# Performance work log

Hardware: AMD Instinct MI355X
Metric: run time of the kernel (lower is better)

The kernel has to match this reference:

```python
import jax, jax.numpy as jnp
from jax import lax
import numpy as np

B, T = 8, 65536
IN_CH, OUT_CH = 1, 2
RES_CH, SKIP_CH = 32, 64
KS, DEPTH, STACKS = 3, 8, 2
L = DEPTH * STACKS
DILATIONS = [2 ** (i % DEPTH) for i in range(L)]


def causal_conv1d(x, w, b, dilation=1):
    # x: (B, Cin, T), w: (Cout, Cin, K) -> (B, Cout, T), left-padded causal
    pad = (w.shape[-1] - 1) * dilation
    out = lax.conv_general_dilated(
        x, w, window_strides=(1,), padding=[(pad, 0)],
        rhs_dilation=(dilation,), dimension_numbers=('NCH', 'OIH', 'NCH'))
    return out + b[None, :, None]


def setup_inputs() -> dict:
    key = jax.random.key(0)
    ks = jax.random.split(key, 16)
    s = 0.05  # small init keeps exp(0.5*log_var) well-behaved
    inp = {
        'x': jax.random.normal(ks[0], (B, IN_CH, T), jnp.float32),
        'W_in': jax.random.normal(ks[1], (L, RES_CH, IN_CH, 1), jnp.float32) * s,
        'b_in': jnp.zeros((L, RES_CH), jnp.float32),
        'W_f': jax.random.normal(ks[2], (L, RES_CH, RES_CH, KS), jnp.float32) * s,
        'b_f': jnp.zeros((L, RES_CH), jnp.float32),
        'W_g': jax.random.normal(ks[3], (L, RES_CH, RES_CH, KS), jnp.float32) * s,
        'b_g': jnp.zeros((L, RES_CH), jnp.float32),
        'W_s': jax.random.normal(ks[4], (L, SKIP_CH, RES_CH, 1), jnp.float32) * s,
        'b_s': jnp.zeros((L, SKIP_CH), jnp.float32),
        'W_o': jax.random.normal(ks[5], (L, IN_CH, RES_CH, 1), jnp.float32) * s,
        'b_o': jnp.zeros((L, IN_CH), jnp.float32),
        'W_sk1': jax.random.normal(ks[6], (SKIP_CH, SKIP_CH, 1), jnp.float32) * s,
        'b_sk1': jnp.zeros((SKIP_CH,), jnp.float32),
        'W_sk2': jax.random.normal(ks[7], (OUT_CH, SKIP_CH, 1), jnp.float32) * s,
        'b_sk2': jnp.zeros((OUT_CH,), jnp.float32),
    }
    return inp


def reference(x, W_in, b_in, W_f, b_f, W_g, b_g, W_s, b_s, W_o, b_o,
              W_sk1, b_sk1, W_sk2, b_sk2):
    out = x
    skip_acc = jnp.zeros((x.shape[0], SKIP_CH, x.shape[2]), x.dtype)
    for i in range(L):
        d = DILATIONS[i]
        residual = causal_conv1d(out, W_in[i], b_in[i])           # (B,res,T)
        f = jnp.tanh(causal_conv1d(residual, W_f[i], b_f[i], d))
        g = jax.nn.sigmoid(causal_conv1d(residual, W_g[i], b_g[i], d))
        gated = f * g
        skip_acc = skip_acc + causal_conv1d(gated, W_s[i], b_s[i])
        out = causal_conv1d(gated, W_o[i], b_o[i]) + out
    skip = jax.nn.relu(causal_conv1d(skip_acc, W_sk1, b_sk1))
    output = causal_conv1d(skip, W_sk2, b_sk2)                    # (B,2,T)
    means = output[:, 0, :]
    stds = jnp.exp(0.5 * output[:, 1, :])
    return means, stds
```

## Files before the change

kernel.cpp:

```cpp
#include <hip/hip_runtime.h>
#include <hip/hip_bf16.h>
#include <math.h>

#define T_LEN 65536
#define B_N   8
#define BT    (T_LEN * B_N)
#define L_N   16
#define RC    32
#define SC    64

#define NT1   256
#define CL    512

#define TS    128

#define A_AF0 0
#define A_AF1 32
#define A_AF2 64
#define A_CF0 96
#define A_CF1 128
#define A_BFC 160
#define A_AG0 192
#define A_AG1 224
#define A_AG2 256
#define A_CG0 288
#define A_CG1 320
#define A_BGC 352
#define A_BFI 384
#define A_BGI 416
#define FW_L  448
#define FW_BSUM (L_N * FW_L)
#define FW_F32  (FW_BSUM + 64)
#define WSBF_N  (L_N * SC * RC)
#define W1BF_N  (SC * SC)

typedef float v2f __attribute__((ext_vector_type(2)));
typedef __attribute__((ext_vector_type(4))) float f4;
typedef __attribute__((ext_vector_type(8))) short bf8;

#define MFMA16(a, b, c) __builtin_amdgcn_mfma_f32_16x16x32_bf16(a, b, c, 0, 0, 0)

__device__ __forceinline__ float fast_rcp(float x) { return __builtin_amdgcn_rcpf(x); }

__device__ __forceinline__ float gated_fn(float fp, float gp) {
    float E = __builtin_amdgcn_exp2f(fp);
    float F = __builtin_amdgcn_exp2f(gp);
    return (E - 1.f) * F * fast_rcp((E + 1.f) * (F + 1.f));
}

__device__ __forceinline__ unsigned short f2bf(float f) {
    unsigned u = __float_as_uint(f);
    u += 0x7fffu + ((u >> 16) & 1u);
    return (unsigned short)(u >> 16);
}

__device__ __forceinline__ unsigned pk2(float lo, float hi) {
    __hip_bfloat162 h = __float22bfloat162_rn(make_float2(lo, hi));
    unsigned u; __builtin_memcpy(&u, &h, 4); return u;
}

__device__ __forceinline__ bf8 mk_bf8(unsigned a, unsigned b, unsigned c, unsigned d) {
    unsigned v[4] = {a, b, c, d};
    bf8 r; __builtin_memcpy(&r, v, 16); return r;
}

__global__ __launch_bounds__(256) void prep_kernel(
    const float* __restrict__ W_f, const float* __restrict__ W_g,
    const float* __restrict__ W_in, const float* __restrict__ b_in,
    const float* __restrict__ b_f, const float* __restrict__ b_g,
    const float* __restrict__ b_s, const float* __restrict__ W_s,
    const float* __restrict__ W_sk1, float* __restrict__ fw,
    short* __restrict__ fwh)
{
    const float SF = 2.88539008177792681472f;
    const float SG = 1.44269504088896340736f;
    int idx = blockIdx.x * 256 + threadIdx.x;
    if (idx < L_N * RC) {
        int i = idx >> 5, c = idx & 31;
        float af[3] = {0,0,0}, cf[3] = {0,0,0}, ag[3] = {0,0,0}, cg[3] = {0,0,0};
        for (int cin = 0; cin < RC; ++cin) {
            float wi = W_in[i * RC + cin];
            float bi = b_in[i * RC + cin];
            #pragma unroll
            for (int k = 0; k < 3; ++k) {
                float wf = W_f[((i * RC + c) * RC + cin) * 3 + k];
                float wg = W_g[((i * RC + c) * RC + cin) * 3 + k];
                af[k] = fmaf(wf, wi, af[k]);
                cf[k] = fmaf(wf, bi, cf[k]);
                ag[k] = fmaf(wg, wi, ag[k]);
                cg[k] = fmaf(wg, bi, cg[k]);
            }
        }
        float* p = fw + i * FW_L;
        p[A_AF0 + c] = af[0] * SF; p[A_AF1 + c] = af[1] * SF; p[A_AF2 + c] = af[2] * SF;
        p[A_CF0 + c] = cf[0] * SF; p[A_CF1 + c] = cf[1] * SF;
        p[A_BFC + c] = (b_f[i * RC + c] + cf[2]) * SF;
        p[A_BFI + c] = (b_f[i * RC + c] + cf[2] + cf[0] + cf[1]) * SF;
        p[A_AG0 + c] = ag[0] * SG; p[A_AG1 + c] = ag[1] * SG; p[A_AG2 + c] = ag[2] * SG;
        p[A_CG0 + c] = cg[0] * SG; p[A_CG1 + c] = cg[1] * SG;
        p[A_BGC + c] = (b_g[i * RC + c] + cg[2]) * SG;
        p[A_BGI + c] = (b_g[i * RC + c] + cg[2] + cg[0] + cg[1]) * SG;
    } else if (idx < L_N * RC + SC) {
        int s = idx - L_N * RC;
        float acc = 0.f;
        for (int i = 0; i < L_N; ++i) acc += b_s[i * SC + s];
        fw[FW_BSUM + s] = acc;
    } else if (idx < 576 + WSBF_N) {
        int j = idx - 576;
        fwh[j] = (short)f2bf(W_s[j]);
    } else if (idx < 576 + WSBF_N + W1BF_N) {
        int j = idx - 576 - WSBF_N;
        fwh[WSBF_N + j] = (short)f2bf(W_sk1[j]);
    }
}

__global__ __launch_bounds__(NT1) void layer_kernel(
    const float* __restrict__ src, float* __restrict__ dst,
    const float* __restrict__ gwl, const float* __restrict__ wol,
    const float* __restrict__ bol, int d)
{
    int b     = blockIdx.x >> 7;
    int chunk = blockIdx.x & 127;
    int t0    = chunk * CL;
    const float* sb = src + (size_t)b * T_LEN;
    float*       db = dst + (size_t)b * T_LEN;
    int tid = threadIdx.x;
    int h   = 2 * d;

    int ta = t0 + tid, tb = ta + NT1;
    v2f s2p, s1p, s0p;
    v2f accp = (v2f){0.f, 0.f};

    if (chunk != 0) {
        s2p.x = sb[ta];     s2p.y = sb[tb];
        s1p.x = sb[ta - d]; s1p.y = sb[tb - d];
        s0p.x = sb[ta - h]; s0p.y = sb[tb - h];
        for (int c4 = 0; c4 < 8; ++c4) {
            f4 vaf0 = *(const f4*)(gwl + A_AF0 + c4 * 4);
            f4 vaf1 = *(const f4*)(gwl + A_AF1 + c4 * 4);
            f4 vaf2 = *(const f4*)(gwl + A_AF2 + c4 * 4);
            f4 vbfi = *(const f4*)(gwl + A_BFI + c4 * 4);
            f4 vag0 = *(const f4*)(gwl + A_AG0 + c4 * 4);
            f4 vag1 = *(const f4*)(gwl + A_AG1 + c4 * 4);
            f4 vag2 = *(const f4*)(gwl + A_AG2 + c4 * 4);
            f4 vbgi = *(const f4*)(gwl + A_BGI + c4 * 4);
            f4 vwo  = *(const f4*)(wol + c4 * 4);
            #pragma unroll
            for (int e = 0; e < 4; ++e) {
                float af0 = vaf0[e], af1 = vaf1[e], af2 = vaf2[e], bfi = vbfi[e];
                float ag0 = vag0[e], ag1 = vag1[e], ag2 = vag2[e], bgi = vbgi[e];
                float woc = vwo[e];
                v2f fp = (v2f){bfi, bfi} + s0p * (v2f){af0, af0} + s1p * (v2f){af1, af1} + s2p * (v2f){af2, af2};
                v2f gp = (v2f){bgi, bgi} + s0p * (v2f){ag0, ag0} + s1p * (v2f){ag1, ag1} + s2p * (v2f){ag2, ag2};
                v2f g;
                g.x = gated_fn(fp.x, gp.x);
                g.y = gated_fn(fp.y, gp.y);
                accp = accp + g * (v2f){woc, woc};
            }
        }
    } else {
        v2f m1p, m0p;
        m1p.x = (ta >= d) ? 1.f : 0.f; m1p.y = (tb >= d) ? 1.f : 0.f;
        m0p.x = (ta >= h) ? 1.f : 0.f; m0p.y = (tb >= h) ? 1.f : 0.f;
        s2p.x = sb[ta];
        s2p.y = sb[tb];
        s1p.x = (ta >= d) ? sb[ta - d] : 0.f;
        s1p.y = (tb >= d) ? sb[tb - d] : 0.f;
        s0p.x = (ta >= h) ? sb[ta - h] : 0.f;
        s0p.y = (tb >= h) ? sb[tb - h] : 0.f;
        for (int c4 = 0; c4 < 8; ++c4) {
            f4 vaf0 = *(const f4*)(gwl + A_AF0 + c4 * 4);
            f4 vaf1 = *(const f4*)(gwl + A_AF1 + c4 * 4);
            f4 vaf2 = *(const f4*)(gwl + A_AF2 + c4 * 4);
            f4 vcf0 = *(const f4*)(gwl + A_CF0 + c4 * 4);
            f4 vcf1 = *(const f4*)(gwl + A_CF1 + c4 * 4);
            f4 vbfc = *(const f4*)(gwl + A_BFC + c4 * 4);
            f4 vag0 = *(const f4*)(gwl + A_AG0 + c4 * 4);
            f4 vag1 = *(const f4*)(gwl + A_AG1 + c4 * 4);
            f4 vag2 = *(const f4*)(gwl + A_AG2 + c4 * 4);
            f4 vcg0 = *(const f4*)(gwl + A_CG0 + c4 * 4);
            f4 vcg1 = *(const f4*)(gwl + A_CG1 + c4 * 4);
            f4 vbgc = *(const f4*)(gwl + A_BGC + c4 * 4);
            f4 vwo  = *(const f4*)(wol + c4 * 4);
            #pragma unroll
            for (int e = 0; e < 4; ++e) {
                float af0 = vaf0[e], af1 = vaf1[e], af2 = vaf2[e];
                float cf0 = vcf0[e], cf1 = vcf1[e], bfc = vbfc[e];
                float ag0 = vag0[e], ag1 = vag1[e], ag2 = vag2[e];
                float cg0 = vcg0[e], cg1 = vcg1[e], bgc = vbgc[e];
                float woc = vwo[e];
                v2f fp = (v2f){bfc, bfc} + m0p * (v2f){cf0, cf0} + m1p * (v2f){cf1, cf1};
                fp = fp + s0p * (v2f){af0, af0} + s1p * (v2f){af1, af1} + s2p * (v2f){af2, af2};
                v2f gp = (v2f){bgc, bgc} + m0p * (v2f){cg0, cg0} + m1p * (v2f){cg1, cg1};
                gp = gp + s0p * (v2f){ag0, ag0} + s1p * (v2f){ag1, ag1} + s2p * (v2f){ag2, ag2};
                v2f g;
                g.x = gated_fn(fp.x, gp.x);
                g.y = gated_fn(fp.y, gp.y);
                accp = accp + g * (v2f){woc, woc};
            }
        }
    }
    float bo = *bol;
    db[ta] = s2p.x + bo + accp.x;
    db[tb] = s2p.y + bo + accp.y;
}

#define SMB_W    0
#define SMB_MISC 28672
#define SMB_TOT  29712

__global__ __launch_bounds__(256) void pass2_kernel(
    const float* __restrict__ x, const float* __restrict__ streams,
    const float* __restrict__ fw, const short* __restrict__ Wsbf,
    const short* __restrict__ W1bf, const float* __restrict__ b_sk1,
    const float* __restrict__ W_sk2, const float* __restrict__ b_sk2,
    float* __restrict__ out)
{
    __shared__ __align__(16) char smb[SMB_TOT];
    float* sW    = (float*)smb;
    float* sMisc = (float*)(smb + SMB_MISC);

    int tid   = threadIdx.x;
    int b     = blockIdx.x >> 9;
    int chunk = blockIdx.x & 511;
    int t0    = chunk * TS;

    for (int j = tid; j < (L_N * FW_L) / 4; j += 256)
        ((f4*)sW)[j] = ((const f4*)fw)[j];
    if (tid < 64) { sMisc[tid] = fw[FW_BSUM + tid]; sMisc[64 + tid] = b_sk1[tid]; }
    if (tid < 128) sMisc[128 + tid] = W_sk2[tid];
    if (tid < 2)   sMisc[256 + tid] = b_sk2[tid];
    __syncthreads();

    int wv   = tid >> 6;
    int lane = tid & 63;
    int m    = lane & 15;
    int q    = lane >> 4;

    int tr0 = t0 + wv * 32 + m;
    int tr1 = tr0 + 16;

    f4 zero4 = {0.f, 0.f, 0.f, 0.f};
    f4 acc[2][4];
    #pragma unroll
    for (int tt = 0; tt < 2; ++tt)
        #pragma unroll
        for (int st = 0; st < 4; ++st) acc[tt][st] = zero4;

    const float* xb = x + (size_t)b * T_LEN;
    for (int i = 0; i < L_N; ++i) {
        int d = 1 << (i & 7);
        const float* src = (i == 0) ? xb
                                    : (streams + (size_t)(i - 1) * BT + (size_t)b * T_LEN);
        const float* w = sW + i * FW_L + q * 8;

        bf8 bfrag[4];
        #pragma unroll
        for (int st = 0; st < 4; ++st)
            bfrag[st] = *(const bf8*)(Wsbf + i * (SC * RC) + (st * 16 + m) * RC + q * 8);

        unsigned uf[2][4];
        if (t0 >= 2 * d) {
            float s2a = src[tr0], s1a = src[tr0 - d], s0a = src[tr0 - 2 * d];
            float s2b = src[tr1], s1b = src[tr1 - d], s0b = src[tr1 - 2 * d];
            #pragma unroll
            for (int hc = 0; hc < 2; ++hc) {
                const float* wc = w + hc * 4;
                f4 af0 = *(const f4*)(wc + A_AF0), af1 = *(const f4*)(wc + A_AF1), af2 = *(const f4*)(wc + A_AF2);
                f4 bfi = *(const f4*)(wc + A_BFI);
                f4 ag0 = *(const f4*)(wc + A_AG0), ag1 = *(const f4*)(wc + A_AG1), ag2 = *(const f4*)(wc + A_AG2);
                f4 bgi = *(const f4*)(wc + A_BGI);
                f4 fpa = bfi + s0a * af0 + s1a * af1 + s2a * af2;
                f4 gpa = bgi + s0a * ag0 + s1a * ag1 + s2a * ag2;
                f4 fpb = bfi + s0b * af0 + s1b * af1 + s2b * af2;
                f4 gpb = bgi + s0b * ag0 + s1b * ag1 + s2b * ag2;
                uf[0][hc * 2 + 0] = pk2(gated_fn(fpa[0], gpa[0]), gated_fn(fpa[1], gpa[1]));
                uf[0][hc * 2 + 1] = pk2(gated_fn(fpa[2], gpa[2]), gated_fn(fpa[3], gpa[3]));
                uf[1][hc * 2 + 0] = pk2(gated_fn(fpb[0], gpb[0]), gated_fn(fpb[1], gpb[1]));
                uf[1][hc * 2 + 1] = pk2(gated_fn(fpb[2], gpb[2]), gated_fn(fpb[3], gpb[3]));
            }
        } else {
            float m1a = (tr0 >= d) ? 1.f : 0.f, m0a = (tr0 >= 2 * d) ? 1.f : 0.f;
            float m1b = (tr1 >= d) ? 1.f : 0.f, m0b = (tr1 >= 2 * d) ? 1.f : 0.f;
            float s2a = src[tr0];
            float s1a = (tr0 >= d)     ? src[tr0 - d]     : 0.f;
            float s0a = (tr0 >= 2 * d) ? src[tr0 - 2 * d] : 0.f;
            float s2b = src[tr1];
            float s1b = (tr1 >= d)     ? src[tr1 - d]     : 0.f;
            float s0b = (tr1 >= 2 * d) ? src[tr1 - 2 * d] : 0.f;
            #pragma unroll
            for (int hc = 0; hc < 2; ++hc) {
                const float* wc = w + hc * 4;
                f4 af0 = *(const f4*)(wc + A_AF0), af1 = *(const f4*)(wc + A_AF1), af2 = *(const f4*)(wc + A_AF2);
                f4 cf0 = *(const f4*)(wc + A_CF0), cf1 = *(const f4*)(wc + A_CF1), bfc = *(const f4*)(wc + A_BFC);
                f4 ag0 = *(const f4*)(wc + A_AG0), ag1 = *(const f4*)(wc + A_AG1), ag2 = *(const f4*)(wc + A_AG2);
                f4 cg0 = *(const f4*)(wc + A_CG0), cg1 = *(const f4*)(wc + A_CG1), bgc = *(const f4*)(wc + A_BGC);
                f4 fpa = bfc + m0a * cf0 + m1a * cf1 + s0a * af0 + s1a * af1 + s2a * af2;
                f4 gpa = bgc + m0a * cg0 + m1a * cg1 + s0a * ag0 + s1a * ag1 + s2a * ag2;
                f4 fpb = bfc + m0b * cf0 + m1b * cf1 + s0b * af0 + s1b * af1 + s2b * af2;
                f4 gpb = bgc + m0b * cg0 + m1b * cg1 + s0b * ag0 + s1b * ag1 + s2b * ag2;
                uf[0][hc * 2 + 0] = pk2(gated_fn(fpa[0], gpa[0]), gated_fn(fpa[1], gpa[1]));
                uf[0][hc * 2 + 1] = pk2(gated_fn(fpa[2], gpa[2]), gated_fn(fpa[3], gpa[3]));
                uf[1][hc * 2 + 0] = pk2(gated_fn(fpb[0], gpb[0]), gated_fn(fpb[1], gpb[1]));
                uf[1][hc * 2 + 1] = pk2(gated_fn(fpb[2], gpb[2]), gated_fn(fpb[3], gpb[3]));
            }
        }

        bf8 a0 = mk_bf8(uf[0][0], uf[0][1], uf[0][2], uf[0][3]);
        bf8 a1 = mk_bf8(uf[1][0], uf[1][1], uf[1][2], uf[1][3]);
        #pragma unroll
        for (int st = 0; st < 4; ++st) {
            acc[0][st] = MFMA16(a0, bfrag[st], acc[0][st]);
            acc[1][st] = MFMA16(a1, bfrag[st], acc[1][st]);
        }
    }

    __syncthreads();
    #pragma unroll
    for (int tt = 0; tt < 2; ++tt) {
        int tb = (wv * 2 + tt) * 16 + q * 4;
        #pragma unroll
        for (int st = 0; st < 4; ++st) {
            int s = st * 16 + m;
            float bs = sMisc[s];
            #pragma unroll
            for (int r = 0; r < 4; ++r)
                *(unsigned short*)(smb + (tb + r) * 144 + s * 2) = f2bf(acc[tt][st][r] + bs);
        }
    }
    bf8 w1f[4][2];
    #pragma unroll
    for (int ot = 0; ot < 4; ++ot)
        #pragma unroll
        for (int kc = 0; kc < 2; ++kc)
            w1f[ot][kc] = *(const bf8*)(W1bf + (ot * 16 + m) * SC + kc * 32 + q * 8);
    __syncthreads();

    f4 hacc[2][4];
    #pragma unroll
    for (int tt = 0; tt < 2; ++tt)
        #pragma unroll
        for (int ot = 0; ot < 4; ++ot) hacc[tt][ot] = zero4;
    #pragma unroll
    for (int tt = 0; tt < 2; ++tt) {
        int trow = (wv * 2 + tt) * 16 + m;
        #pragma unroll
        for (int kc = 0; kc < 2; ++kc) {
            bf8 afrag = *(const bf8*)(smb + trow * 144 + kc * 64 + q * 16);
            #pragma unroll
            for (int ot = 0; ot < 4; ++ot)
                hacc[tt][ot] = MFMA16(afrag, w1f[ot][kc], hacc[tt][ot]);
        }
    }

    float p0[2][4], p1[2][4];
    #pragma unroll
    for (int tt = 0; tt < 2; ++tt)
        #pragma unroll
        for (int r = 0; r < 4; ++r) { p0[tt][r] = 0.f; p1[tt][r] = 0.f; }
    #pragma unroll
    for (int ot = 0; ot < 4; ++ot) {
        int o = ot * 16 + m;
        float w20 = sMisc[128 + o], w21 = sMisc[192 + o], b1v = sMisc[64 + o];
        #pragma unroll
        for (int tt = 0; tt < 2; ++tt)
            #pragma unroll
            for (int r = 0; r < 4; ++r) {
                float hv = fmaxf(hacc[tt][ot][r] + b1v, 0.f);
                p0[tt][r] = fmaf(w20, hv, p0[tt][r]);
                p1[tt][r] = fmaf(w21, hv, p1[tt][r]);
            }
    }
    #pragma unroll
    for (int msk = 1; msk <= 8; msk <<= 1) {
        #pragma unroll
        for (int tt = 0; tt < 2; ++tt)
            #pragma unroll
            for (int r = 0; r < 4; ++r) {
                p0[tt][r] += __shfl_xor(p0[tt][r], msk);
                p1[tt][r] += __shfl_xor(p1[tt][r], msk);
            }
    }
    if (m == 0) {
        float b20 = sMisc[256], b21 = sMisc[257];
        #pragma unroll
        for (int tt = 0; tt < 2; ++tt) {
            int t = t0 + (wv * 2 + tt) * 16 + q * 4;
            size_t gi = (size_t)b * T_LEN + t;
            f4 mv, sv;
            #pragma unroll
            for (int r = 0; r < 4; ++r) {
                mv[r] = p0[tt][r] + b20;
                sv[r] = __expf(0.5f * (p1[tt][r] + b21));
            }
            *(f4*)(out + gi)      = mv;
            *(f4*)(out + BT + gi) = sv;
        }
    }
}

extern "C" void kernel_launch(void* const* d_in, const int* in_sizes, int n_in,
                              void* d_out, int out_size, void* d_ws, size_t ws_size,
                              hipStream_t stream) {
    const float* x     = (const float*)d_in[0];
    const float* W_in  = (const float*)d_in[1];
    const float* b_in  = (const float*)d_in[2];
    const float* W_f   = (const float*)d_in[3];
    const float* b_f   = (const float*)d_in[4];
    const float* W_g   = (const float*)d_in[5];
    const float* b_g   = (const float*)d_in[6];
    const float* W_s   = (const float*)d_in[7];
    const float* b_s   = (const float*)d_in[8];
    const float* W_o   = (const float*)d_in[9];
    const float* b_o   = (const float*)d_in[10];
    const float* W_sk1 = (const float*)d_in[11];
    const float* b_sk1 = (const float*)d_in[12];
    const float* W_sk2 = (const float*)d_in[13];
    const float* b_sk2 = (const float*)d_in[14];
    float* outp = (float*)d_out;

    float* streams = (float*)d_ws;
    float* fw      = streams + (size_t)15 * BT;
    short* fwh     = (short*)(fw + FW_F32);

    int prep_items = 576 + WSBF_N + W1BF_N;
    prep_kernel<<<(prep_items + 255) / 256, 256, 0, stream>>>(
        W_f, W_g, W_in, b_in, b_f, b_g, b_s, W_s, W_sk1, fw, fwh);
    for (int i = 0; i < 15; ++i) {
        int d = 1 << (i & 7);
        const float* src = (i == 0) ? x : streams + (size_t)(i - 1) * BT;
        layer_kernel<<<B_N * (T_LEN / CL), NT1, 0, stream>>>(
            src, streams + (size_t)i * BT, fw + i * FW_L, W_o + i * 32, b_o + i, d);
    }
    pass2_kernel<<<B_N * (T_LEN / TS), 256, 0, stream>>>(
        x, streams, fw, fwh, fwh + WSBF_N, b_sk1, W_sk2, b_sk2, outp);
}
```

Baseline: 410.2 us.

## Halve layer chunk to one sample per thread; compact pass2 weights and prefetch next-layer inputs

The layer kernel now handles one time sample per thread with chunk length 256, doubling the grid so there are more blocks for latency hiding and fewer registers per thread. Pass2 loads a compact interior-only weight table into shared memory, which cuts LDS use so more blocks can be resident. For chunks with no boundary masking, pass2 loads the next layer's stream values one iteration ahead to hide global load latency. Boundary chunks fall back to reading the full weight table directly from global memory. The cost is more blocks and a duplicated code path.

```diff
diff --git a/kernel.cpp b/kernel.cpp
--- a/kernel.cpp
+++ b/kernel.cpp
@@ -10,7 +10,7 @@
 #define SC    64
 
 #define NT1   256
-#define CL    512
+#define CL    256
 
 #define TS    128
 
@@ -34,6 +34,17 @@
 #define WSBF_N  (L_N * SC * RC)
 #define W1BF_N  (SC * SC)
 
+#define B_AF0 0
+#define B_AF1 32
+#define B_AF2 64
+#define B_BFI 96
+#define B_AG0 128
+#define B_AG1 160
+#define B_AG2 192
+#define B_BGI 224
+#define IW_L  256
+#define FWI_F32 (L_N * IW_L)
+
 typedef float v2f __attribute__((ext_vector_type(2)));
 typedef __attribute__((ext_vector_type(4))) float f4;
 typedef __attribute__((ext_vector_type(8))) short bf8;
@@ -70,7 +81,7 @@
     const float* __restrict__ b_f, const float* __restrict__ b_g,
     const float* __restrict__ b_s, const float* __restrict__ W_s,
     const float* __restrict__ W_sk1, float* __restrict__ fw,
-    short* __restrict__ fwh)
+    short* __restrict__ fwh, float* __restrict__ fwi)
 {
     const float SF = 2.88539008177792681472f;
     const float SG = 1.44269504088896340736f;
@@ -100,6 +111,11 @@
         p[A_CG0 + c] = cg[0] * SG; p[A_CG1 + c] = cg[1] * SG;
         p[A_BGC + c] = (b_g[i * RC + c] + cg[2]) * SG;
         p[A_BGI + c] = (b_g[i * RC + c] + cg[2] + cg[0] + cg[1]) * SG;
+        float* pi = fwi + i * IW_L;
+        pi[B_AF0 + c] = af[0] * SF; pi[B_AF1 + c] = af[1] * SF; pi[B_AF2 + c] = af[2] * SF;
+        pi[B_BFI + c] = (b_f[i * RC + c] + cf[2] + cf[0] + cf[1]) * SF;
+        pi[B_AG0 + c] = ag[0] * SG; pi[B_AG1 + c] = ag[1] * SG; pi[B_AG2 + c] = ag[2] * SG;
+        pi[B_BGI + c] = (b_g[i * RC + c] + cg[2] + cg[0] + cg[1]) * SG;
     } else if (idx < L_N * RC + SC) {
         int s = idx - L_N * RC;
         float acc = 0.f;
@@ -119,22 +135,20 @@
     const float* __restrict__ gwl, const float* __restrict__ wol,
     const float* __restrict__ bol, int d)
 {
-    int b     = blockIdx.x >> 7;
-    int chunk = blockIdx.x & 127;
+    int b     = blockIdx.x >> 8;
+    int chunk = blockIdx.x & 255;
     int t0    = chunk * CL;
     const float* sb = src + (size_t)b * T_LEN;
     float*       db = dst + (size_t)b * T_LEN;
     int tid = threadIdx.x;
     int h   = 2 * d;
 
-    int ta = t0 + tid, tb = ta + NT1;
-    v2f s2p, s1p, s0p;
-    v2f accp = (v2f){0.f, 0.f};
+    int ta = t0 + tid;
+    float s2, s1, s0;
+    float acc = 0.f;
 
     if (chunk != 0) {
-        s2p.x = sb[ta];     s2p.y = sb[tb];
-        s1p.x = sb[ta - d]; s1p.y = sb[tb - d];
-        s0p.x = sb[ta - h]; s0p.y = sb[tb - h];
+        s2 = sb[ta]; s1 = sb[ta - d]; s0 = sb[ta - h];
         for (int c4 = 0; c4 < 8; ++c4) {
             f4 vaf0 = *(const f4*)(gwl + A_AF0 + c4 * 4);
             f4 vaf1 = *(const f4*)(gwl + A_AF1 + c4 * 4);
@@ -147,27 +161,17 @@
             f4 vwo  = *(const f4*)(wol + c4 * 4);
             #pragma unroll
             for (int e = 0; e < 4; ++e) {
-                float af0 = vaf0[e], af1 = vaf1[e], af2 = vaf2[e], bfi = vbfi[e];
-                float ag0 = vag0[e], ag1 = vag1[e], ag2 = vag2[e], bgi = vbgi[e];
-                float woc = vwo[e];
-                v2f fp = (v2f){bfi, bfi} + s0p * (v2f){af0, af0} + s1p * (v2f){af1, af1} + s2p * (v2f){af2, af2};
-                v2f gp = (v2f){bgi, bgi} + s0p * (v2f){ag0, ag0} + s1p * (v2f){ag1, ag1} + s2p * (v2f){ag2, ag2};
-                v2f g;
-                g.x = gated_fn(fp.x, gp.x);
-                g.y = gated_fn(fp.y, gp.y);
-                accp = accp + g * (v2f){woc, woc};
+                float fp = vbfi[e] + s0 * vaf0[e] + s1 * vaf1[e] + s2 * vaf2[e];
+                float gp = vbgi[e] + s0 * vag0[e] + s1 * vag1[e] + s2 * vag2[e];
+                acc = fmaf(gated_fn(fp, gp), vwo[e], acc);
             }
         }
     } else {
-        v2f m1p, m0p;
-        m1p.x = (ta >= d) ? 1.f : 0.f; m1p.y = (tb >= d) ? 1.f : 0.f;
-        m0p.x = (ta >= h) ? 1.f : 0.f; m0p.y = (tb >= h) ? 1.f : 0.f;
-        s2p.x = sb[ta];
-        s2p.y = sb[tb];
-        s1p.x = (ta >= d) ? sb[ta - d] : 0.f;
-        s1p.y = (tb >= d) ? sb[tb - d] : 0.f;
-        s0p.x = (ta >= h) ? sb[ta - h] : 0.f;
-        s0p.y = (tb >= h) ? sb[tb - h] : 0.f;
+        float m1 = (ta >= d) ? 1.f : 0.f;
+        float m0 = (ta >= h) ? 1.f : 0.f;
+        s2 = sb[ta];
+        s1 = (ta >= d) ? sb[ta - d] : 0.f;
+        s0 = (ta >= h) ? sb[ta - h] : 0.f;
         for (int c4 = 0; c4 < 8; ++c4) {
             f4 vaf0 = *(const f4*)(gwl + A_AF0 + c4 * 4);
             f4 vaf1 = *(const f4*)(gwl + A_AF1 + c4 * 4);
@@ -184,37 +188,26 @@
             f4 vwo  = *(const f4*)(wol + c4 * 4);
             #pragma unroll
             for (int e = 0; e < 4; ++e) {
-                float af0 = vaf0[e], af1 = vaf1[e], af2 = vaf2[e];
-                float cf0 = vcf0[e], cf1 = vcf1[e], bfc = vbfc[e];
-                float ag0 = vag0[e], ag1 = vag1[e], ag2 = vag2[e];
-                float cg0 = vcg0[e], cg1 = vcg1[e], bgc = vbgc[e];
-                float woc = vwo[e];
-                v2f fp = (v2f){bfc, bfc} + m0p * (v2f){cf0, cf0} + m1p * (v2f){cf1, cf1};
-                fp = fp + s0p * (v2f){af0, af0} + s1p * (v2f){af1, af1} + s2p * (v2f){af2, af2};
-                v2f gp = (v2f){bgc, bgc} + m0p * (v2f){cg0, cg0} + m1p * (v2f){cg1, cg1};
-                gp = gp + s0p * (v2f){ag0, ag0} + s1p * (v2f){ag1, ag1} + s2p * (v2f){ag2, ag2};
-                v2f g;
-                g.x = gated_fn(fp.x, gp.x);
-                g.y = gated_fn(fp.y, gp.y);
-                accp = accp + g * (v2f){woc, woc};
-            }
-        }
-    }
-    float bo = *bol;
-    db[ta] = s2p.x + bo + accp.x;
-    db[tb] = s2p.y + bo + accp.y;
-}
-
-#define SMB_W    0
-#define SMB_MISC 28672
-#define SMB_TOT  29712
+                float fp = vbfc[e] + m0 * vcf0[e] + m1 * vcf1[e]
+                         + s0 * vaf0[e] + s1 * vaf1[e] + s2 * vaf2[e];
+                float gp = vbgc[e] + m0 * vcg0[e] + m1 * vcg1[e]
+                         + s0 * vag0[e] + s1 * vag1[e] + s2 * vag2[e];
+                acc = fmaf(gated_fn(fp, gp), vwo[e], acc);
+            }
+        }
+    }
+    db[ta] = s2 + *bol + acc;
+}
+
+#define SMB_MISC 18432
+#define SMB_TOT  19472
 
 __global__ __launch_bounds__(256) void pass2_kernel(
     const float* __restrict__ x, const float* __restrict__ streams,
-    const float* __restrict__ fw, const short* __restrict__ Wsbf,
-    const short* __restrict__ W1bf, const float* __restrict__ b_sk1,
-    const float* __restrict__ W_sk2, const float* __restrict__ b_sk2,
-    float* __restrict__ out)
+    const float* __restrict__ fw, const float* __restrict__ fwi,
+    const short* __restrict__ Wsbf, const short* __restrict__ W1bf,
+    const float* __restrict__ b_sk1, const float* __restrict__ W_sk2,
+    const float* __restrict__ b_sk2, float* __restrict__ out)
 {
     __shared__ __align__(16) char smb[SMB_TOT];
     float* sW    = (float*)smb;
@@ -225,8 +218,8 @@
     int chunk = blockIdx.x & 511;
     int t0    = chunk * TS;
 
-    for (int j = tid; j < (L_N * FW_L) / 4; j += 256)
-        ((f4*)sW)[j] = ((const f4*)fw)[j];
+    for (int j = tid; j < FWI_F32 / 4; j += 256)
+        ((f4*)sW)[j] = ((const f4*)fwi)[j];
     if (tid < 64) { sMisc[tid] = fw[FW_BSUM + tid]; sMisc[64 + tid] = b_sk1[tid]; }
     if (tid < 128) sMisc[128 + tid] = W_sk2[tid];
     if (tid < 2)   sMisc[256 + tid] = b_sk2[tid];
@@ -248,70 +241,121 @@
         for (int st = 0; st < 4; ++st) acc[tt][st] = zero4;
 
     const float* xb = x + (size_t)b * T_LEN;
-    for (int i = 0; i < L_N; ++i) {
-        int d = 1 << (i & 7);
-        const float* src = (i == 0) ? xb
-                                    : (streams + (size_t)(i - 1) * BT + (size_t)b * T_LEN);
-        const float* w = sW + i * FW_L + q * 8;
-
-        bf8 bfrag[4];
-        #pragma unroll
-        for (int st = 0; st < 4; ++st)
-            bfrag[st] = *(const bf8*)(Wsbf + i * (SC * RC) + (st * 16 + m) * RC + q * 8);
-
-        unsigned uf[2][4];
-        if (t0 >= 2 * d) {
-            float s2a = src[tr0], s1a = src[tr0 - d], s0a = src[tr0 - 2 * d];
-            float s2b = src[tr1], s1b = src[tr1 - d], s0b = src[tr1 - 2 * d];
+
+    if (chunk >= 2) {
+        float c2a = xb[tr0], c1a = xb[tr0 - 1], c0a = xb[tr0 - 2];
+        float c2b = xb[tr1], c1b = xb[tr1 - 1], c0b = xb[tr1 - 2];
+        for (int i = 0; i < L_N; ++i) {
+            float n2a, n1a, n0a, n2b, n1b, n0b;
+            if (i + 1 < L_N) {
+                int dn = 1 << ((i + 1) & 7);
+                const float* sn = streams + (size_t)i * BT + (size_t)b * T_LEN;
+                n2a = sn[tr0]; n1a = sn[tr0 - dn]; n0a = sn[tr0 - 2 * dn];
+                n2b = sn[tr1]; n1b = sn[tr1 - dn]; n0b = sn[tr1 - 2 * dn];
+            } else {
+                n2a = n1a = n0a = n2b = n1b = n0b = 0.f;
+            }
+
+            bf8 bfrag[4];
+            #pragma unroll
+            for (int st = 0; st < 4; ++st)
+                bfrag[st] = *(const bf8*)(Wsbf + i * (SC * RC) + (st * 16 + m) * RC + q * 8);
+
+            const float* w = sW + i * IW_L + q * 8;
+            unsigned uf[2][4];
             #pragma unroll
             for (int hc = 0; hc < 2; ++hc) {
                 const float* wc = w + hc * 4;
-                f4 af0 = *(const f4*)(wc + A_AF0), af1 = *(const f4*)(wc + A_AF1), af2 = *(const f4*)(wc + A_AF2);
-                f4 bfi = *(const f4*)(wc + A_BFI);
-                f4 ag0 = *(const f4*)(wc + A_AG0), ag1 = *(const f4*)(wc + A_AG1), ag2 = *(const f4*)(wc + A_AG2);
-                f4 bgi = *(const f4*)(wc + A_BGI);
-                f4 fpa = bfi + s0a * af0 + s1a * af1 + s2a * af2;
-                f4 gpa = bgi + s0a * ag0 + s1a * ag1 + s2a * ag2;
-                f4 fpb = bfi + s0b * af0 + s1b * af1 + s2b * af2;
-                f4 gpb = bgi + s0b * ag0 + s1b * ag1 + s2b * ag2;
+                f4 af0 = *(const f4*)(wc + B_AF0), af1 = *(const f4*)(wc + B_AF1), af2 = *(const f4*)(wc + B_AF2);
+                f4 bfi = *(const f4*)(wc + B_BFI);
+                f4 ag0 = *(const f4*)(wc + B_AG0), ag1 = *(const f4*)(wc + B_AG1), ag2 = *(const f4*)(wc + B_AG2);
+                f4 bgi = *(const f4*)(wc + B_BGI);
+                f4 fpa = bfi + c0a * af0 + c1a * af1 + c2a * af2;
+                f4 gpa = bgi + c0a * ag0 + c1a * ag1 + c2a * ag2;
+                f4 fpb = bfi + c0b * af0 + c1b * af1 + c2b * af2;
+                f4 gpb = bgi + c0b * ag0 + c1b * ag1 + c2b * ag2;
                 uf[0][hc * 2 + 0] = pk2(gated_fn(fpa[0], gpa[0]), gated_fn(fpa[1], gpa[1]));
                 uf[0][hc * 2 + 1] = pk2(gated_fn(fpa[2], gpa[2]), gated_fn(fpa[3], gpa[3]));
                 uf[1][hc * 2 + 0] = pk2(gated_fn(fpb[0], gpb[0]), gated_fn(fpb[1], gpb[1]));
                 uf[1][hc * 2 + 1] = pk2(gated_fn(fpb[2], gpb[2]), gated_fn(fpb[3], gpb[3]));
             }
-        } else {
-            float m1a = (tr0 >= d) ? 1.f : 0.f, m0a = (tr0 >= 2 * d) ? 1.f : 0.f;
-            float m1b = (tr1 >= d) ? 1.f : 0.f, m0b = (tr1 >= 2 * d) ? 1.f : 0.f;
-            float s2a = src[tr0];
-            float s1a = (tr0 >= d)     ? src[tr0 - d]     : 0.f;
-            float s0a = (tr0 >= 2 * d) ? src[tr0 - 2 * d] : 0.f;
-            float s2b = src[tr1];
-            float s1b = (tr1 >= d)     ? src[tr1 - d]     : 0.f;
-            float s0b = (tr1 >= 2 * d) ? src[tr1 - 2 * d] : 0.f;
-            #pragma unroll
-            for (int hc = 0; hc < 2; ++hc) {
-                const float* wc = w + hc * 4;
-                f4 af0 = *(const f4*)(wc + A_AF0), af1 = *(const f4*)(wc + A_AF1), af2 = *(const f4*)(wc + A_AF2);
-                f4 cf0 = *(const f4*)(wc + A_CF0), cf1 = *(const f4*)(wc + A_CF1), bfc = *(const f4*)(wc + A_BFC);
-                f4 ag0 = *(const f4*)(wc + A_AG0), ag1 = *(const f4*)(wc + A_AG1), ag2 = *(const f4*)(wc + A_AG2);
-                f4 cg0 = *(const f4*)(wc + A_CG0), cg1 = *(const f4*)(wc + A_CG1), bgc = *(const f4*)(wc + A_BGC);
-                f4 fpa = bfc + m0a * cf0 + m1a * cf1 + s0a * af0 + s1a * af1 + s2a * af2;
-                f4 gpa = bgc + m0a * cg0 + m1a * cg1 + s0a * ag0 + s1a * ag1 + s2a * ag2;
-                f4 fpb = bfc + m0b * cf0 + m1b * cf1 + s0b * af0 + s1b * af1 + s2b * af2;
-                f4 gpb = bgc + m0b * cg0 + m1b * cg1 + s0b * ag0 + s1b * ag1 + s2b * ag2;
-                uf[0][hc * 2 + 0] = pk2(gated_fn(fpa[0], gpa[0]), gated_fn(fpa[1], gpa[1]));
-                uf[0][hc * 2 + 1] = pk2(gated_fn(fpa[2], gpa[2]), gated_fn(fpa[3], gpa[3]));
-                uf[1][hc * 2 + 0] = pk2(gated_fn(fpb[0], gpb[0]), gated_fn(fpb[1], gpb[1]));
-                uf[1][hc * 2 + 1] = pk2(gated_fn(fpb[2], gpb[2]), gated_fn(fpb[3], gpb[3]));
-            }
-        }
-
-        bf8 a0 = mk_bf8(uf[0][0], uf[0][1], uf[0][2], uf[0][3]);
-        bf8 a1 = mk_bf8(uf[1][0], uf[1][1], uf[1][2], uf[1][3]);
-        #pragma unroll
-        for (int st = 0; st < 4; ++st) {
-            acc[0][st] = MFMA16(a0, bfrag[st], acc[0][st]);
-            acc[1][st] = MFMA16(a1, bfrag[st], acc[1][st]);
+
+            bf8 a0 = mk_bf8(uf[0][0], uf[0][1], uf[0][2], uf[0][3]);
+            bf8 a1 = mk_bf8(uf[1][0], uf[1][1], uf[1][2], uf[1][3]);
+            #pragma unroll
+            for (int st = 0; st < 4; ++st) {
+                acc[0][st] = MFMA16(a0, bfrag[st], acc[0][st]);
+                acc[1][st] = MFMA16(a1, bfrag[st], acc[1][st]);
+            }
+            c2a = n2a; c1a = n1a; c0a = n0a;
+            c2b = n2b; c1b = n1b; c0b = n0b;
+        }
+    } else {
+        for (int i = 0; i < L_N; ++i) {
+            int d = 1 << (i & 7);
+            const float* src = (i == 0) ? xb
+                                        : (streams + (size_t)(i - 1) * BT + (size_t)b * T_LEN);
+            const float* w = fw + i * FW_L + q * 8;
+
+            bf8 bfrag[4];
+            #pragma unroll
+            for (int st = 0; st < 4; ++st)
+                bfrag[st] = *(const bf8*)(Wsbf + i * (SC * RC) + (st * 16 + m) * RC + q * 8);
+
+            unsigned uf[2][4];
+            if (t0 >= 2 * d) {
+                float s2a = src[tr0], s1a = src[tr0 - d], s0a = src[tr0 - 2 * d];
+                float s2b = src[tr1], s1b = src[tr1 - d], s0b = src[tr1 - 2 * d];
+                #pragma unroll
+                for (int hc = 0; hc < 2; ++hc) {
+                    const float* wc = w + hc * 4;
+                    f4 af0 = *(const f4*)(wc + A_AF0), af1 = *(const f4*)(wc + A_AF1), af2 = *(const f4*)(wc + A_AF2);
+                    f4 bfi = *(const f4*)(wc + A_BFI);
+                    f4 ag0 = *(const f4*)(wc + A_AG0), ag1 = *(const f4*)(wc + A_AG1), ag2 = *(const f4*)(wc + A_AG2);
+                    f4 bgi = *(const f4*)(wc + A_BGI);
+                    f4 fpa = bfi + s0a * af0 + s1a * af1 + s2a * af2;
+                    f4 gpa = bgi + s0a * ag0 + s1a * ag1 + s2a * ag2;
+                    f4 fpb = bfi + s0b * af0 + s1b * af1 + s2b * af2;
+                    f4 gpb = bgi + s0b * ag0 + s1b * ag1 + s2b * ag2;
+                    uf[0][hc * 2 + 0] = pk2(gated_fn(fpa[0], gpa[0]), gated_fn(fpa[1], gpa[1]));
+                    uf[0][hc * 2 + 1] = pk2(gated_fn(fpa[2], gpa[2]), gated_fn(fpa[3], gpa[3]));
+                    uf[1][hc * 2 + 0] = pk2(gated_fn(fpb[0], gpb[0]), gated_fn(fpb[1], gpb[1]));
+                    uf[1][hc * 2 + 1] = pk2(gated_fn(fpb[2], gpb[2]), gated_fn(fpb[3], gpb[3]));
+                }
+            } else {
+                float m1a = (tr0 >= d) ? 1.f : 0.f, m0a = (tr0 >= 2 * d) ? 1.f : 0.f;
+                float m1b = (tr1 >= d) ? 1.f : 0.f, m0b = (tr1 >= 2 * d) ? 1.f : 0.f;
+                float s2a = src[tr0];
+                float s1a = (tr0 >= d)     ? src[tr0 - d]     : 0.f;
+                float s0a = (tr0 >= 2 * d) ? src[tr0 - 2 * d] : 0.f;
+                float s2b = src[tr1];
+                float s1b = (tr1 >= d)     ? src[tr1 - d]     : 0.f;
+                float s0b = (tr1 >= 2 * d) ? src[tr1 - 2 * d] : 0.f;
+                #pragma unroll
+                for (int hc = 0; hc < 2; ++hc) {
+                    const float* wc = w + hc * 4;
+                    f4 af0 = *(const f4*)(wc + A_AF0), af1 = *(const f4*)(wc + A_AF1), af2 = *(const f4*)(wc + A_AF2);
+                    f4 cf0 = *(const f4*)(wc + A_CF0), cf1 = *(const f4*)(wc + A_CF1), bfc = *(const f4*)(wc + A_BFC);
+                    f4 ag0 = *(const f4*)(wc + A_AG0), ag1 = *(const f4*)(wc + A_AG1), ag2 = *(const f4*)(wc + A_AG2);
+                    f4 cg0 = *(const f4*)(wc + A_CG0), cg1 = *(const f4*)(wc + A_CG1), bgc = *(const f4*)(wc + A_BGC);
+                    f4 fpa = bfc + m0a * cf0 + m1a * cf1 + s0a * af0 + s1a * af1 + s2a * af2;
+                    f4 gpa = bgc + m0a * cg0 + m1a * cg1 + s0a * ag0 + s1a * ag1 + s2a * ag2;
+                    f4 fpb = bfc + m0b * cf0 + m1b * cf1 + s0b * af0 + s1b * af1 + s2b * af2;
+                    f4 gpb = bgc + m0b * cg0 + m1b * cg1 + s0b * ag0 + s1b * ag1 + s2b * ag2;
+                    uf[0][hc * 2 + 0] = pk2(gated_fn(fpa[0], gpa[0]), gated_fn(fpa[1], gpa[1]));
+                    uf[0][hc * 2 + 1] = pk2(gated_fn(fpa[2], gpa[2]), gated_fn(fpa[3], gpa[3]));
+                    uf[1][hc * 2 + 0] = pk2(gated_fn(fpb[0], gpb[0]), gated_fn(fpb[1], gpb[1]));
+                    uf[1][hc * 2 + 1] = pk2(gated_fn(fpb[2], gpb[2]), gated_fn(fpb[3], gpb[3]));
+                }
+            }
+
+            bf8 a0 = mk_bf8(uf[0][0], uf[0][1], uf[0][2], uf[0][3]);
+            bf8 a1 = mk_bf8(uf[1][0], uf[1][1], uf[1][2], uf[1][3]);
+            #pragma unroll
+            for (int st = 0; st < 4; ++st) {
+                acc[0][st] = MFMA16(a0, bfrag[st], acc[0][st]);
+                acc[1][st] = MFMA16(a1, bfrag[st], acc[1][st]);
+            }
         }
     }
 
@@ -422,10 +466,11 @@
     float* streams = (float*)d_ws;
     float* fw      = streams + (size_t)15 * BT;
     short* fwh     = (short*)(fw + FW_F32);
+    float* fwi     = (float*)(fwh + WSBF_N + W1BF_N);
 
     int prep_items = 576 + WSBF_N + W1BF_N;
     prep_kernel<<<(prep_items + 255) / 256, 256, 0, stream>>>(
-        W_f, W_g, W_in, b_in, b_f, b_g, b_s, W_s, W_sk1, fw, fwh);
+        W_f, W_g, W_in, b_in, b_f, b_g, b_s, W_s, W_sk1, fw, fwh, fwi);
     for (int i = 0; i < 15; ++i) {
         int d = 1 << (i & 7);
         const float* src = (i == 0) ? x : streams + (size_t)(i - 1) * BT;
@@ -433,5 +478,5 @@
             src, streams + (size_t)i * BT, fw + i * FW_L, W_o + i * 32, b_o + i, d);
     }
     pass2_kernel<<<B_N * (T_LEN / TS), 256, 0, stream>>>(
-        x, streams, fw, fwh, fwh + WSBF_N, b_sk1, W_sk2, b_sk2, outp);
-}
+        x, streams, fw, fwi, fwh, fwh + WSBF_N, b_sk1, W_sk2, b_sk2, outp);
+}
```

After: 447.7 us. 9.1% more time.
